# Optimization experiments

Hardware: AMD Instinct MI355X
Metric: run time of the kernel (lower is better)

Reference implementation:

```python
import jax, jax.numpy as jnp
import numpy as np

EMBED_DIM = 512
NUM_HEADS = 8
HEAD_DIM = EMBED_DIM // NUM_HEADS
BATCH = 2
SEQ = 4096
LN_EPS = 1e-5


def setup_inputs() -> dict:
    key = jax.random.key(0)
    ks = jax.random.split(key, 10)
    s = 1.0 / np.sqrt(EMBED_DIM)
    d = dict(
        x=jax.random.normal(ks[0], (BATCH, SEQ, EMBED_DIM), dtype=jnp.float32),
        wq=jax.random.normal(ks[1], (EMBED_DIM, EMBED_DIM), dtype=jnp.float32) * s,
        bq=jnp.zeros((EMBED_DIM,), jnp.float32),
        wk=jax.random.normal(ks[2], (EMBED_DIM, EMBED_DIM), dtype=jnp.float32) * s,
        bk=jnp.zeros((EMBED_DIM,), jnp.float32),
        wv=jax.random.normal(ks[3], (EMBED_DIM, EMBED_DIM), dtype=jnp.float32) * s,
        bv=jnp.zeros((EMBED_DIM,), jnp.float32),
        wo=jax.random.normal(ks[4], (EMBED_DIM, EMBED_DIM), dtype=jnp.float32) * s,
        bo=jnp.zeros((EMBED_DIM,), jnp.float32),
        ln_g=jnp.ones((EMBED_DIM,), jnp.float32),
        ln_b=jnp.zeros((EMBED_DIM,), jnp.float32),
    )
    return d


def reference(x, wq, bq, wk, bk, wv, bv, wo, bo, ln_g, ln_b):
    B, S, E = x.shape
    H, D = NUM_HEADS, HEAD_DIM
    residual = x
    # QKV projections (weights stored [in, out])
    q = (x @ wq + bq).reshape(B, S, H, D).transpose(0, 2, 1, 3)  # [B,H,S,D]
    k = (x @ wk + bk).reshape(B, S, H, D).transpose(0, 2, 1, 3)
    v = (x @ wv + bv).reshape(B, S, H, D).transpose(0, 2, 1, 3)
    # scaled dot-product attention
    scores = jnp.einsum('bhsd,bhtd->bhst', q, k) / jnp.sqrt(jnp.float32(D))
    attn = jax.nn.softmax(scores, axis=-1)
    ctx = jnp.einsum('bhst,bhtd->bhsd', attn, v)  # [B,H,S,D]
    ctx = ctx.transpose(0, 2, 1, 3).reshape(B, S, E)
    # output projection (dropout=0 in eval) + residual + LayerNorm
    out = ctx @ wo + bo
    y = out + residual
    mu = jnp.mean(y, axis=-1, keepdims=True)
    var = jnp.var(y, axis=-1, keepdims=True)
    y = (y - mu) * jax.lax.rsqrt(var + LN_EPS) * ln_g + ln_b
    return y
```

## Files before the change

kernel.cpp:

```cpp
#include <hip/hip_runtime.h>


typedef unsigned short u16;
typedef unsigned int u32;
typedef short bf16x8 __attribute__((ext_vector_type(8)));
typedef float f32x2 __attribute__((ext_vector_type(2)));
typedef float f32x4 __attribute__((ext_vector_type(4)));
typedef float f32x8 __attribute__((ext_vector_type(8)));
typedef float f32x16 __attribute__((ext_vector_type(16)));
typedef unsigned short u16x4 __attribute__((ext_vector_type(4)));
typedef unsigned int u32x2 __attribute__((ext_vector_type(2)));
typedef unsigned int u32x4 __attribute__((ext_vector_type(4)));

#define S_LEN 4096
#define E_DIM 512
#define H_NUM 8
#define D_DIM 64
#define M_ROWS 8192

#define Q_SCALE 0.18033688011112042f

static __device__ __forceinline__ u16 f2bf(float f) {
    unsigned int u = __float_as_uint(f);
    u += 0x7fffu + ((u >> 16) & 1u);
    return (u16)(u >> 16);
}

static __device__ __forceinline__ u32 cvt_pk_bf16(float a, float b) {
    u32 r;
    asm("v_cvt_pk_bf16_f32 %0, %1, %2" : "=v"(r) : "v"(a), "v"(b));
    return r;
}

#if __has_builtin(__builtin_amdgcn_exp2f)
#define EXP2(x) __builtin_amdgcn_exp2f(x)
#else
static __device__ __forceinline__ float exp2_hw(float x) {
    float r;
    asm volatile("v_exp_f32 %0, %1\n\ts_nop 1" : "=v"(r) : "v"(x));
    return r;
}
#define EXP2(x) exp2_hw(x)
#endif

static __device__ __forceinline__ float vsum16(f32x16 v) {
    f32x8 a = __builtin_shufflevector(v, v, 0, 1, 2, 3, 4, 5, 6, 7) +
              __builtin_shufflevector(v, v, 8, 9, 10, 11, 12, 13, 14, 15);
    f32x4 b = __builtin_shufflevector(a, a, 0, 1, 2, 3) +
              __builtin_shufflevector(a, a, 4, 5, 6, 7);
    f32x2 c = __builtin_shufflevector(b, b, 0, 1) +
              __builtin_shufflevector(b, b, 2, 3);
    return c[0] + c[1];
}

static __device__ __forceinline__ void gload_lds16(const u16* g, u16* l) {
    __builtin_amdgcn_global_load_lds(
        (const __attribute__((address_space(1))) u32*)g,
        (__attribute__((address_space(3))) u32*)l, 16, 0, 0);
}

__global__ __launch_bounds__(256) void cvt_all_k(
    const float* __restrict__ x, u16* __restrict__ xb,
    const float* __restrict__ w0, const float* __restrict__ w1,
    const float* __restrict__ w2, const float* __restrict__ w3,
    u16* __restrict__ o0, u16* __restrict__ o1,
    u16* __restrict__ o2, u16* __restrict__ o3)
{
    __shared__ float fT[64][68];
    if (blockIdx.x < 4096) {
        int i = blockIdx.x * 256 + threadIdx.x;
        float4 v = ((const float4*)x)[i];
        u16x4 o;
        o[0] = f2bf(v.x); o[1] = f2bf(v.y); o[2] = f2bf(v.z); o[3] = f2bf(v.w);
        ((u16x4*)xb)[i] = o;
        return;
    }
    const int g = blockIdx.x - 4096;
    const int which = g >> 6;
    const int tile = g & 63;
    const int k0 = (tile >> 3) * 64, n0 = (tile & 7) * 64;
    const float* w = which == 0 ? w0 : which == 1 ? w1 : which == 2 ? w2 : w3;
    u16* o = which == 0 ? o0 : which == 1 ? o1 : which == 2 ? o2 : o3;
    const int tr = threadIdx.x >> 4, tc = threadIdx.x & 15;
    #pragma unroll
    for (int p = 0; p < 4; p++) {
        const int kr = p * 16 + tr;
        float4 v = *(const float4*)&w[(size_t)(k0 + kr) * 512 + n0 + tc * 4];
        fT[tc * 4 + 0][kr] = v.x;
        fT[tc * 4 + 1][kr] = v.y;
        fT[tc * 4 + 2][kr] = v.z;
        fT[tc * 4 + 3][kr] = v.w;
    }
    __syncthreads();
    #pragma unroll
    for (int p = 0; p < 4; p++) {
        const int nr = p * 16 + tr;
        u16x4 ov;
        ov[0] = f2bf(fT[nr][tc * 4 + 0]);
        ov[1] = f2bf(fT[nr][tc * 4 + 1]);
        ov[2] = f2bf(fT[nr][tc * 4 + 2]);
        ov[3] = f2bf(fT[nr][tc * 4 + 3]);
        *(u16x4*)&o[(size_t)(n0 + nr) * 512 + k0 + tc * 4] = ov;
    }
}

template <int BM, int BN>
__global__ __launch_bounds__(256) void qkv_k(
    const u16* __restrict__ A,
    const u16* __restrict__ Wt0, const u16* __restrict__ Wt1,
    const u16* __restrict__ Wt2,
    const float* __restrict__ b0, const float* __restrict__ b1,
    const float* __restrict__ b2,
    u16* __restrict__ q_out, u16* __restrict__ k_out, u16* __restrict__ vt_out)
{
    constexpr int FM = BM / 32, FN = BN / 32;
    __shared__ __align__(16) u16 Asm[BM * 32];
    __shared__ __align__(16) u16 Bsm[BN * 32];

    const int t = threadIdx.x, wave = t >> 6, lane = t & 63;
    constexpr int nb_per = 512 / BN;
    const int sel = blockIdx.x / nb_per, bn = blockIdx.x % nb_per;
    const int bm = blockIdx.y;

    const u16* Wt = sel == 0 ? Wt0 : (sel == 1 ? Wt1 : Wt2);
    const float* bias = sel == 0 ? b0 : (sel == 1 ? b1 : b2);

    const int wm = (wave >> 1) * (BM / 2);
    const int wn = (wave & 1) * (BN / 2);
    const int lrow = lane & 15, kq = (lane >> 4) * 8;

    f32x4 acc[FM][FN];
    #pragma unroll
    for (int i = 0; i < FM; i++)
        #pragma unroll
        for (int j = 0; j < FN; j++)
            acc[i][j] = (f32x4){0.f, 0.f, 0.f, 0.f};

    const u16* Ag = A + (size_t)bm * BM * 512 + (size_t)(t >> 2) * 512 + (t & 3) * 8;
    const u16* Bg = Wt + (size_t)bn * BN * 512 + (size_t)(t >> 2) * 512 + (t & 3) * 8;
    u16* Al = Asm + (size_t)wave * 512;
    u16* Bl = Bsm + (size_t)wave * 512;

    for (int kk = 0; kk < 512; kk += 32) {
        #pragma unroll
        for (int p = 0; p < BM / 64; p++)
            gload_lds16(Ag + (size_t)p * 64 * 512 + kk, Al + p * 2048);
        #pragma unroll
        for (int p = 0; p < BN / 64; p++)
            gload_lds16(Bg + (size_t)p * 64 * 512 + kk, Bl + p * 2048);
        __syncthreads();

        bf16x8 af[FM], bfv[FN];
        #pragma unroll
        for (int i = 0; i < FM; i++)
            af[i] = *(const bf16x8*)&Asm[(wm + i * 16 + lrow) * 32 + kq];
        #pragma unroll
        for (int j = 0; j < FN; j++)
            bfv[j] = *(const bf16x8*)&Bsm[(wn + j * 16 + lrow) * 32 + kq];
        #pragma unroll
        for (int i = 0; i < FM; i++)
            #pragma unroll
            for (int j = 0; j < FN; j++)
                acc[i][j] = __builtin_amdgcn_mfma_f32_16x16x32_bf16(
                    af[i], bfv[j], acc[i][j], 0, 0, 0);
        __syncthreads();
    }

    #pragma unroll
    for (int i = 0; i < FM; i++) {
        #pragma unroll
        for (int j = 0; j < FN; j++) {
            const int col = bn * BN + wn + j * 16 + lrow;
            const float bcol = bias[col];
            const int row0 = bm * BM + wm + i * 16 + (lane >> 4) * 4;
            const int b = row0 >> 12, s0v = row0 & 4095;
            const int h = col >> 6,  d = col & 63;
            if (sel == 2) {
                u16x4 pk;
                #pragma unroll
                for (int q = 0; q < 4; q++)
                    pk[q] = f2bf(acc[i][j][q] + bcol);
                *(u16x4*)&vt_out[(((size_t)(b * 8 + h)) * 64 + d) * 4096 + s0v] = pk;
            } else {
                u16* o = (sel == 0) ? q_out : k_out;
                const float sc = (sel == 0) ? Q_SCALE : 1.0f;
                #pragma unroll
                for (int q = 0; q < 4; q++)
                    o[(((size_t)(b * 8 + h)) * 4096 + s0v + q) * 64 + d] =
                        f2bf((acc[i][j][q] + bcol) * sc);
            }
        }
    }
}

__global__ __launch_bounds__(256) void oproj_ln_k(
    const u16* __restrict__ A,
    const u16* __restrict__ Wt,
    const float* __restrict__ bo,
    const float* __restrict__ x,
    const float* __restrict__ g, const float* __restrict__ beta,
    float* __restrict__ out)
{
    __shared__ __align__(16) u16 Asm[32 * 32];
    __shared__ __align__(16) u16 Bsm[512 * 32];
    __shared__ float red[4][32][2];

    const int t = threadIdx.x, wave = t >> 6, lane = t & 63;
    const int lrow = lane & 15, kq4 = (lane >> 4) * 4, kq = (lane >> 4) * 8;
    const int wn = wave * 128;
    const int bm = blockIdx.x;

    f32x4 acc[2][8];
    #pragma unroll
    for (int i = 0; i < 2; i++)
        #pragma unroll
        for (int j = 0; j < 8; j++)
            acc[i][j] = (f32x4){0.f, 0.f, 0.f, 0.f};

    const u16* Ag = A + (size_t)bm * 32 * 512 + (size_t)(t >> 2) * 512 + (t & 3) * 8;
    const u16* Bg = Wt + (size_t)(t >> 2) * 512 + (t & 3) * 8;
    u16* Al = Asm + (size_t)wave * 512;
    u16* Bl = Bsm + (size_t)wave * 512;

    for (int kk = 0; kk < 512; kk += 32) {
        if (t < 128) gload_lds16(Ag + kk, Al);
        #pragma unroll
        for (int p = 0; p < 8; p++)
            gload_lds16(Bg + (size_t)p * 64 * 512 + kk, Bl + p * 2048);
        __syncthreads();

        bf16x8 af[2], bfv[8];
        #pragma unroll
        for (int i = 0; i < 2; i++)
            af[i] = *(const bf16x8*)&Asm[(i * 16 + lrow) * 32 + kq];
        #pragma unroll
        for (int j = 0; j < 8; j++)
            bfv[j] = *(const bf16x8*)&Bsm[(wn + j * 16 + lrow) * 32 + kq];
        #pragma unroll
        for (int i = 0; i < 2; i++)
            #pragma unroll
            for (int j = 0; j < 8; j++)
                acc[i][j] = __builtin_amdgcn_mfma_f32_16x16x32_bf16(
                    af[i], bfv[j], acc[i][j], 0, 0, 0);
        __syncthreads();
    }

    const int grow0 = bm * 32;
    #pragma unroll
    for (int i = 0; i < 2; i++) {
        #pragma unroll
        for (int q = 0; q < 4; q++) {
            const int rl = i * 16 + kq4 + q;
            float s = 0.f, ss = 0.f;
            #pragma unroll
            for (int j = 0; j < 8; j++) {
                const int col = wn + j * 16 + lrow;
                float v = acc[i][j][q] + bo[col] +
                          x[(size_t)(grow0 + rl) * 512 + col];
                acc[i][j][q] = v;
                s += v; ss += v * v;
            }
            s  += __shfl_xor(s, 1);  ss += __shfl_xor(ss, 1);
            s  += __shfl_xor(s, 2);  ss += __shfl_xor(ss, 2);
            s  += __shfl_xor(s, 4);  ss += __shfl_xor(ss, 4);
            s  += __shfl_xor(s, 8);  ss += __shfl_xor(ss, 8);
            if (lrow == 0) { red[wave][rl][0] = s; red[wave][rl][1] = ss; }
        }
    }
    __syncthreads();

    #pragma unroll
    for (int i = 0; i < 2; i++) {
        #pragma unroll
        for (int q = 0; q < 4; q++) {
            const int rl = i * 16 + kq4 + q;
            const float srow = red[0][rl][0] + red[1][rl][0] +
                               red[2][rl][0] + red[3][rl][0];
            const float ssrow = red[0][rl][1] + red[1][rl][1] +
                                red[2][rl][1] + red[3][rl][1];
            const float mu = srow * (1.0f / 512.0f);
            const float var = ssrow * (1.0f / 512.0f) - mu * mu;
            const float inv = rsqrtf(var + 1e-5f);
            #pragma unroll
            for (int j = 0; j < 8; j++) {
                const int col = wn + j * 16 + lrow;
                out[(size_t)(grow0 + rl) * 512 + col] =
                    (acc[i][j][q] - mu) * inv * g[col] + beta[col];
            }
        }
    }
}

__global__ __launch_bounds__(512, 2) void attn_k(
    const u16* __restrict__ Q, const u16* __restrict__ K,
    const u16* __restrict__ Vt, u16* __restrict__ ctx)
{
    __shared__ __align__(16) u16 SM[32768];

    const int t = threadIdx.x, w = t >> 6, lane = t & 63;
    const int l31 = lane & 31, hi = lane >> 5;
    const int kh = w >> 2, wl = w & 3;

    const int bid = blockIdx.x;
    const int xcd = bid & 7, j = bid >> 3;
    const int head = xcd * 2 + (j & 1);
    const int qt = j >> 1;

    const u16* Qb = Q + (size_t)head * S_LEN * D_DIM;
    const u16* Kb = K + (size_t)head * S_LEN * D_DIM;
    const u16* Vb = Vt + (size_t)head * D_DIM * S_LEN;
    const int q0w = qt * 256 + wl * 64;

    bf16x8 qfA[4], qfB[4];
    #pragma unroll
    for (int ks = 0; ks < 4; ks++) {
        qfA[ks] = *(const bf16x8*)&Qb[(size_t)(q0w + l31) * 64 + ks * 16 + hi * 8];
        qfB[ks] = *(const bf16x8*)&Qb[(size_t)(q0w + 32 + l31) * 64 + ks * 16 + hi * 8];
    }

    u16* const KH = SM + kh * 16384;
    u16* const VH = KH + 8192;

    const u16* kp[8];
    const u16* vp[8];
    #pragma unroll
    for (int i = 0; i < 8; i++) {
        const int r = (i >> 2) * 32 + l31;
        const int c = (i & 3) * 2 + hi;
        const int phys = r * 8 + (c ^ (r & 7));
        kp[i] = KH + phys * 8;
        vp[i] = VH + phys * 8;
    }

    f32x16 acc0A = {0.f}, acc1A = {0.f}, acc0B = {0.f}, acc1B = {0.f};
    float lA = 0.f, lB = 0.f;
    f32x16 sCA, sCB, sNA, sNB;
    bf16x8 pfA[2], pfB[2];

    const int th = t & 255;
    const int c0 = th, c1 = th + 256;
    const int sr0 = c0 >> 3, sc0 = (c0 & 7) ^ (sr0 & 7);
    const int sr1 = c1 >> 3, sc1 = (c1 & 7) ^ (sr1 & 7);
    const u16* kg0 = Kb + (size_t)(kh * 2048 + sr0) * 64 + sc0 * 8;
    const u16* kg1 = Kb + (size_t)(kh * 2048 + sr1) * 64 + sc1 * 8;
    const u16* vg0 = Vb + (size_t)sr0 * S_LEN + kh * 2048 + sc0 * 8;
    const u16* vg1 = Vb + (size_t)sr1 * S_LEN + kh * 2048 + sc1 * 8;
    u16* const kd0 = KH + wl * 512;
    u16* const kd1 = KH + 2048 + wl * 512;
    u16* const vd0 = VH + wl * 512;
    u16* const vd1 = VH + 2048 + wl * 512;

#define ATTN_STAGE(DST)                                                      \
    {                                                                        \
        gload_lds16(kg0, kd0 + (DST)); gload_lds16(kg1, kd1 + (DST));        \
        gload_lds16(vg0, vd0 + (DST)); gload_lds16(vg1, vd1 + (DST));        \
        kg0 += 4096; kg1 += 4096; vg0 += 64; vg1 += 64;                      \
    }

#define QK_H(BUF, H, SA, SB)                                                 \
    {                                                                        \
        SA = (f32x16){0.f}; SB = (f32x16){0.f};                              \
        __builtin_amdgcn_s_setprio(1);                                       \
        _Pragma("unroll")                                                    \
        for (int ks = 0; ks < 4; ks++) {                                     \
            bf16x8 ka = *(const bf16x8*)(kp[4 * (H) + ks] + (BUF));          \
            SA = __builtin_amdgcn_mfma_f32_32x32x16_bf16(ka, qfA[ks], SA, 0, 0, 0); \
            SB = __builtin_amdgcn_mfma_f32_32x32x16_bf16(ka, qfB[ks], SB, 0, 0, 0); \
        }                                                                    \
        __builtin_amdgcn_s_setprio(0);                                       \
    }

#define EXPPACK_H(SA, SB)                                                    \
    {                                                                        \
        _Pragma("unroll")                                                    \
        for (int e = 0; e < 16; e++) {                                       \
            SA[e] = EXP2(SA[e]); SB[e] = EXP2(SB[e]);                        \
        }                                                                    \
        lA += vsum16(SA);                                                    \
        lB += vsum16(SB);                                                    \
        _Pragma("unroll")                                                    \
        for (int jx = 0; jx < 2; jx++) {                                     \
            const int r0 = jx * 8;                                           \
            u32 ax1 = cvt_pk_bf16(SA[r0 + 0], SA[r0 + 1]);                   \
            u32 ay1 = cvt_pk_bf16(SA[r0 + 4], SA[r0 + 5]);                   \
            asm("v_permlane32_swap_b32 %0, %1" : "+v"(ax1), "+v"(ay1));      \
            u32 ax2 = cvt_pk_bf16(SA[r0 + 2], SA[r0 + 3]);                   \
            u32 ay2 = cvt_pk_bf16(SA[r0 + 6], SA[r0 + 7]);                   \
            asm("v_permlane32_swap_b32 %0, %1" : "+v"(ax2), "+v"(ay2));      \
            u32x4 wva; wva[0] = ax1; wva[1] = ax2; wva[2] = ay1; wva[3] = ay2; \
            pfA[jx] = *(bf16x8*)&wva;                                        \
            u32 bx1 = cvt_pk_bf16(SB[r0 + 0], SB[r0 + 1]);                   \
            u32 by1 = cvt_pk_bf16(SB[r0 + 4], SB[r0 + 5]);                   \
            asm("v_permlane32_swap_b32 %0, %1" : "+v"(bx1), "+v"(by1));      \
            u32 bx2 = cvt_pk_bf16(SB[r0 + 2], SB[r0 + 3]);                   \
            u32 by2 = cvt_pk_bf16(SB[r0 + 6], SB[r0 + 7]);                   \
            asm("v_permlane32_swap_b32 %0, %1" : "+v"(bx2), "+v"(by2));      \
            u32x4 wvb; wvb[0] = bx1; wvb[1] = bx2; wvb[2] = by1; wvb[3] = by2; \
            pfB[jx] = *(bf16x8*)&wvb;                                        \
        }                                                                    \
    }

#define PV_H(BUF, H)                                                         \
    {                                                                        \
        __builtin_amdgcn_s_setprio(1);                                       \
        _Pragma("unroll")                                                    \
        for (int jx = 0; jx < 2; jx++) {                                     \
            bf16x8 va = *(const bf16x8*)(vp[2 * (H) + jx] + (BUF));          \
            bf16x8 vb2 = *(const bf16x8*)(vp[4 + 2 * (H) + jx] + (BUF));     \
            acc0A = __builtin_amdgcn_mfma_f32_32x32x16_bf16(va, pfA[jx], acc0A, 0, 0, 0); \
            acc0B = __builtin_amdgcn_mfma_f32_32x32x16_bf16(va, pfB[jx], acc0B, 0, 0, 0); \
            acc1A = __builtin_amdgcn_mfma_f32_32x32x16_bf16(vb2, pfA[jx], acc1A, 0, 0, 0); \
            acc1B = __builtin_amdgcn_mfma_f32_32x32x16_bf16(vb2, pfB[jx], acc1B, 0, 0, 0); \
        }                                                                    \
        __builtin_amdgcn_s_setprio(0);                                       \
    }

#define BODY(BUF, NBUF, LAST)                                                \
    {                                                                        \
        if (!(LAST)) ATTN_STAGE(NBUF);                                       \
        if (w & 1) {                                                         \
            EXPPACK_H(sCA, sCB);                                             \
            QK_H(BUF, 1, sNA, sNB);                                          \
        } else {                                                             \
            QK_H(BUF, 1, sNA, sNB);                                          \
            EXPPACK_H(sCA, sCB);                                             \
        }                                                                    \
        PV_H(BUF, 0);                                                        \
        EXPPACK_H(sNA, sNB);                                                 \
        PV_H(BUF, 1);                                                        \
        __syncthreads();                                                     \
        if (!(LAST)) QK_H(NBUF, 0, sCA, sCB);                                \
    }

    ATTN_STAGE(0);
    __syncthreads();
    QK_H(0, 0, sCA, sCB);

    for (int it = 0; it < 15; ++it) {
        BODY(0, 4096, 0);
        BODY(4096, 0, 0);
    }
    BODY(0, 4096, 0);
    BODY(4096, 0, 1);

    __syncthreads();
    float* const cb = (float*)SM;
    float* const p = cb + (size_t)(wl * 64 + lane) * 34;
    if (kh == 1) {
        #pragma unroll
        for (int e = 0; e < 16; e++) { p[e] = acc0A[e]; p[16 + e] = acc0B[e]; }
        p[32] = lA; p[33] = lB;
    }
    __syncthreads();
    if (kh == 0) {
        #pragma unroll
        for (int e = 0; e < 16; e++) { acc0A[e] += p[e]; acc0B[e] += p[16 + e]; }
        lA += p[32]; lB += p[33];
    }
    __syncthreads();
    if (kh == 1) {
        #pragma unroll
        for (int e = 0; e < 16; e++) { p[e] = acc1A[e]; p[16 + e] = acc1B[e]; }
    }
    __syncthreads();
    if (kh == 0) {
        #pragma unroll
        for (int e = 0; e < 16; e++) { acc1A[e] += p[e]; acc1B[e] += p[16 + e]; }
        lA += __shfl_xor(lA, 32);
        lB += __shfl_xor(lB, 32);

        const int b = head >> 3, h = head & 7;
        const float liA = 1.0f / lA, liB = 1.0f / lB;
        const size_t oA = (size_t)(b * S_LEN + q0w + l31) * 512 + h * 64 + 4 * hi;
        const size_t oB = oA + (size_t)32 * 512;
        #pragma unroll
        for (int rq = 0; rq < 4; rq++) {
            u32x2 wa;
            wa[0] = cvt_pk_bf16(acc0A[4 * rq + 0] * liA, acc0A[4 * rq + 1] * liA);
            wa[1] = cvt_pk_bf16(acc0A[4 * rq + 2] * liA, acc0A[4 * rq + 3] * liA);
            *(u32x2*)&ctx[oA + 8 * rq] = wa;
            wa[0] = cvt_pk_bf16(acc1A[4 * rq + 0] * liA, acc1A[4 * rq + 1] * liA);
            wa[1] = cvt_pk_bf16(acc1A[4 * rq + 2] * liA, acc1A[4 * rq + 3] * liA);
            *(u32x2*)&ctx[oA + 32 + 8 * rq] = wa;
            wa[0] = cvt_pk_bf16(acc0B[4 * rq + 0] * liB, acc0B[4 * rq + 1] * liB);
            wa[1] = cvt_pk_bf16(acc0B[4 * rq + 2] * liB, acc0B[4 * rq + 3] * liB);
            *(u32x2*)&ctx[oB + 8 * rq] = wa;
            wa[0] = cvt_pk_bf16(acc1B[4 * rq + 0] * liB, acc1B[4 * rq + 1] * liB);
            wa[1] = cvt_pk_bf16(acc1B[4 * rq + 2] * liB, acc1B[4 * rq + 3] * liB);
            *(u32x2*)&ctx[oB + 32 + 8 * rq] = wa;
        }
    }
#undef ATTN_STAGE
#undef QK_H
#undef EXPPACK_H
#undef PV_H
#undef BODY
}

extern "C" void kernel_launch(void* const* d_in, const int* in_sizes, int n_in,
                              void* d_out, int out_size, void* d_ws, size_t ws_size,
                              hipStream_t stream)
{
    const float* x    = (const float*)d_in[0];
    const float* wq   = (const float*)d_in[1];
    const float* bq   = (const float*)d_in[2];
    const float* wk   = (const float*)d_in[3];
    const float* bk   = (const float*)d_in[4];
    const float* wv   = (const float*)d_in[5];
    const float* bv   = (const float*)d_in[6];
    const float* wo   = (const float*)d_in[7];
    const float* bo   = (const float*)d_in[8];
    const float* ln_g = (const float*)d_in[9];
    const float* ln_b = (const float*)d_in[10];

    char* ws = (char*)d_ws;
    u16* xb   = (u16*)(ws);
    u16* wqt  = (u16*)(ws + 8388608);
    u16* wkt  = (u16*)(ws + 8912896);
    u16* wvt  = (u16*)(ws + 9437184);
    u16* wot  = (u16*)(ws + 9961472);
    u16* Qb   = (u16*)(ws + 10485760);
    u16* Kb   = (u16*)(ws + 18874368);
    u16* Vtb  = (u16*)(ws + 27262976);
    u16* ctxb = (u16*)(ws + 35651584);

    cvt_all_k<<<4352, 256, 0, stream>>>(x, xb, wq, wk, wv, wo,
                                        wqt, wkt, wvt, wot);

    qkv_k<128, 128><<<dim3(12, 64), 256, 0, stream>>>(
        xb, wqt, wkt, wvt, bq, bk, bv, Qb, Kb, Vtb);

    attn_k<<<256, 512, 0, stream>>>(Qb, Kb, Vtb, ctxb);

    oproj_ln_k<<<256, 256, 0, stream>>>(ctxb, wot, bo, x, ln_g, ln_b,
                                        (float*)d_out);
}
```

Baseline: 140.2 us.

## Halve attention query tile per block and double QKV GEMM k-step

The attention kernel now gives each wave 32 query rows instead of 64 and launches 512 blocks instead of 256. This halves register accumulators and raises parallelism, but K/V tiles are reloaded twice as often per query and the per-wave odd/even interleave of exp and QK is dropped. The QKV GEMM now stages two 32-wide k-chunks per barrier pair, halving the number of syncs at the cost of doubling its LDS footprint. The attention launch bound drops the minimum of two blocks per CU.

```diff
diff --git a/kernel.cpp b/kernel.cpp
--- a/kernel.cpp
+++ b/kernel.cpp
@@ -114,8 +114,8 @@
     u16* __restrict__ q_out, u16* __restrict__ k_out, u16* __restrict__ vt_out)
 {
     constexpr int FM = BM / 32, FN = BN / 32;
-    __shared__ __align__(16) u16 Asm[BM * 32];
-    __shared__ __align__(16) u16 Bsm[BN * 32];
+    __shared__ __align__(16) u16 Asm[2 * BM * 32];
+    __shared__ __align__(16) u16 Bsm[2 * BN * 32];
 
     const int t = threadIdx.x, wave = t >> 6, lane = t & 63;
     constexpr int nb_per = 512 / BN;
@@ -141,28 +141,38 @@
     u16* Al = Asm + (size_t)wave * 512;
     u16* Bl = Bsm + (size_t)wave * 512;
 
-    for (int kk = 0; kk < 512; kk += 32) {
-        #pragma unroll
-        for (int p = 0; p < BM / 64; p++)
-            gload_lds16(Ag + (size_t)p * 64 * 512 + kk, Al + p * 2048);
-        #pragma unroll
-        for (int p = 0; p < BN / 64; p++)
-            gload_lds16(Bg + (size_t)p * 64 * 512 + kk, Bl + p * 2048);
+    for (int kk = 0; kk < 512; kk += 64) {
+        #pragma unroll
+        for (int c = 0; c < 2; c++) {
+            #pragma unroll
+            for (int p = 0; p < BM / 64; p++)
+                gload_lds16(Ag + (size_t)p * 64 * 512 + kk + c * 32,
+                            Al + c * (BM * 32) + p * 2048);
+            #pragma unroll
+            for (int p = 0; p < BN / 64; p++)
+                gload_lds16(Bg + (size_t)p * 64 * 512 + kk + c * 32,
+                            Bl + c * (BN * 32) + p * 2048);
+        }
         __syncthreads();
 
-        bf16x8 af[FM], bfv[FN];
-        #pragma unroll
-        for (int i = 0; i < FM; i++)
-            af[i] = *(const bf16x8*)&Asm[(wm + i * 16 + lrow) * 32 + kq];
-        #pragma unroll
-        for (int j = 0; j < FN; j++)
-            bfv[j] = *(const bf16x8*)&Bsm[(wn + j * 16 + lrow) * 32 + kq];
-        #pragma unroll
-        for (int i = 0; i < FM; i++)
+        #pragma unroll
+        for (int c = 0; c < 2; c++) {
+            bf16x8 af[FM], bfv[FN];
+            #pragma unroll
+            for (int i = 0; i < FM; i++)
+                af[i] = *(const bf16x8*)
+                    &Asm[c * (BM * 32) + (wm + i * 16 + lrow) * 32 + kq];
             #pragma unroll
             for (int j = 0; j < FN; j++)
-                acc[i][j] = __builtin_amdgcn_mfma_f32_16x16x32_bf16(
-                    af[i], bfv[j], acc[i][j], 0, 0, 0);
+                bfv[j] = *(const bf16x8*)
+                    &Bsm[c * (BN * 32) + (wn + j * 16 + lrow) * 32 + kq];
+            #pragma unroll
+            for (int i = 0; i < FM; i++)
+                #pragma unroll
+                for (int j = 0; j < FN; j++)
+                    acc[i][j] = __builtin_amdgcn_mfma_f32_16x16x32_bf16(
+                        af[i], bfv[j], acc[i][j], 0, 0, 0);
+        }
         __syncthreads();
     }
 
@@ -291,7 +301,7 @@
     }
 }
 
-__global__ __launch_bounds__(512, 2) void attn_k(
+__global__ __launch_bounds__(512) void attn_k(
     const u16* __restrict__ Q, const u16* __restrict__ K,
     const u16* __restrict__ Vt, u16* __restrict__ ctx)
 {
@@ -309,14 +319,12 @@
     const u16* Qb = Q + (size_t)head * S_LEN * D_DIM;
     const u16* Kb = K + (size_t)head * S_LEN * D_DIM;
     const u16* Vb = Vt + (size_t)head * D_DIM * S_LEN;
-    const int q0w = qt * 256 + wl * 64;
-
-    bf16x8 qfA[4], qfB[4];
-    #pragma unroll
-    for (int ks = 0; ks < 4; ks++) {
-        qfA[ks] = *(const bf16x8*)&Qb[(size_t)(q0w + l31) * 64 + ks * 16 + hi * 8];
-        qfB[ks] = *(const bf16x8*)&Qb[(size_t)(q0w + 32 + l31) * 64 + ks * 16 + hi * 8];
-    }
+    const int q0w = qt * 128 + wl * 32;
+
+    bf16x8 qf[4];
+    #pragma unroll
+    for (int ks = 0; ks < 4; ks++)
+        qf[ks] = *(const bf16x8*)&Qb[(size_t)(q0w + l31) * 64 + ks * 16 + hi * 8];
 
     u16* const KH = SM + kh * 16384;
     u16* const VH = KH + 8192;
@@ -332,10 +340,10 @@
         vp[i] = VH + phys * 8;
     }
 
-    f32x16 acc0A = {0.f}, acc1A = {0.f}, acc0B = {0.f}, acc1B = {0.f};
-    float lA = 0.f, lB = 0.f;
-    f32x16 sCA, sCB, sNA, sNB;
-    bf16x8 pfA[2], pfB[2];
+    f32x16 acc0 = {0.f}, acc1 = {0.f};
+    float l = 0.f;
+    f32x16 sC, sN;
+    bf16x8 pf[2];
 
     const int th = t & 255;
     const int c0 = th, c1 = th + 256;
@@ -357,46 +365,34 @@
         kg0 += 4096; kg1 += 4096; vg0 += 64; vg1 += 64;                      \
     }
 
-#define QK_H(BUF, H, SA, SB)                                                 \
+#define QK_H(BUF, H, S)                                                      \
     {                                                                        \
-        SA = (f32x16){0.f}; SB = (f32x16){0.f};                              \
+        S = (f32x16){0.f};                                                   \
         __builtin_amdgcn_s_setprio(1);                                       \
         _Pragma("unroll")                                                    \
         for (int ks = 0; ks < 4; ks++) {                                     \
             bf16x8 ka = *(const bf16x8*)(kp[4 * (H) + ks] + (BUF));          \
-            SA = __builtin_amdgcn_mfma_f32_32x32x16_bf16(ka, qfA[ks], SA, 0, 0, 0); \
-            SB = __builtin_amdgcn_mfma_f32_32x32x16_bf16(ka, qfB[ks], SB, 0, 0, 0); \
+            S = __builtin_amdgcn_mfma_f32_32x32x16_bf16(ka, qf[ks], S, 0, 0, 0); \
         }                                                                    \
         __builtin_amdgcn_s_setprio(0);                                       \
     }
 
-#define EXPPACK_H(SA, SB)                                                    \
+#define EXPPACK_H(S)                                                         \
     {                                                                        \
         _Pragma("unroll")                                                    \
-        for (int e = 0; e < 16; e++) {                                       \
-            SA[e] = EXP2(SA[e]); SB[e] = EXP2(SB[e]);                        \
-        }                                                                    \
-        lA += vsum16(SA);                                                    \
-        lB += vsum16(SB);                                                    \
+        for (int e = 0; e < 16; e++) S[e] = EXP2(S[e]);                      \
+        l += vsum16(S);                                                      \
         _Pragma("unroll")                                                    \
         for (int jx = 0; jx < 2; jx++) {                                     \
             const int r0 = jx * 8;                                           \
-            u32 ax1 = cvt_pk_bf16(SA[r0 + 0], SA[r0 + 1]);                   \
-            u32 ay1 = cvt_pk_bf16(SA[r0 + 4], SA[r0 + 5]);                   \
-            asm("v_permlane32_swap_b32 %0, %1" : "+v"(ax1), "+v"(ay1));      \
-            u32 ax2 = cvt_pk_bf16(SA[r0 + 2], SA[r0 + 3]);                   \
-            u32 ay2 = cvt_pk_bf16(SA[r0 + 6], SA[r0 + 7]);                   \
-            asm("v_permlane32_swap_b32 %0, %1" : "+v"(ax2), "+v"(ay2));      \
-            u32x4 wva; wva[0] = ax1; wva[1] = ax2; wva[2] = ay1; wva[3] = ay2; \
-            pfA[jx] = *(bf16x8*)&wva;                                        \
-            u32 bx1 = cvt_pk_bf16(SB[r0 + 0], SB[r0 + 1]);                   \
-            u32 by1 = cvt_pk_bf16(SB[r0 + 4], SB[r0 + 5]);                   \
-            asm("v_permlane32_swap_b32 %0, %1" : "+v"(bx1), "+v"(by1));      \
-            u32 bx2 = cvt_pk_bf16(SB[r0 + 2], SB[r0 + 3]);                   \
-            u32 by2 = cvt_pk_bf16(SB[r0 + 6], SB[r0 + 7]);                   \
-            asm("v_permlane32_swap_b32 %0, %1" : "+v"(bx2), "+v"(by2));      \
-            u32x4 wvb; wvb[0] = bx1; wvb[1] = bx2; wvb[2] = by1; wvb[3] = by2; \
-            pfB[jx] = *(bf16x8*)&wvb;                                        \
+            u32 x1 = cvt_pk_bf16(S[r0 + 0], S[r0 + 1]);                      \
+            u32 y1 = cvt_pk_bf16(S[r0 + 4], S[r0 + 5]);                      \
+            asm("v_permlane32_swap_b32 %0, %1" : "+v"(x1), "+v"(y1));        \
+            u32 x2 = cvt_pk_bf16(S[r0 + 2], S[r0 + 3]);                      \
+            u32 y2 = cvt_pk_bf16(S[r0 + 6], S[r0 + 7]);                      \
+            asm("v_permlane32_swap_b32 %0, %1" : "+v"(x2), "+v"(y2));        \
+            u32x4 wv; wv[0] = x1; wv[1] = x2; wv[2] = y1; wv[3] = y2;        \
+            pf[jx] = *(bf16x8*)&wv;                                          \
         }                                                                    \
     }
 
@@ -407,10 +403,8 @@
         for (int jx = 0; jx < 2; jx++) {                                     \
             bf16x8 va = *(const bf16x8*)(vp[2 * (H) + jx] + (BUF));          \
             bf16x8 vb2 = *(const bf16x8*)(vp[4 + 2 * (H) + jx] + (BUF));     \
-            acc0A = __builtin_amdgcn_mfma_f32_32x32x16_bf16(va, pfA[jx], acc0A, 0, 0, 0); \
-            acc0B = __builtin_amdgcn_mfma_f32_32x32x16_bf16(va, pfB[jx], acc0B, 0, 0, 0); \
-            acc1A = __builtin_amdgcn_mfma_f32_32x32x16_bf16(vb2, pfA[jx], acc1A, 0, 0, 0); \
-            acc1B = __builtin_amdgcn_mfma_f32_32x32x16_bf16(vb2, pfB[jx], acc1B, 0, 0, 0); \
+            acc0 = __builtin_amdgcn_mfma_f32_32x32x16_bf16(va, pf[jx], acc0, 0, 0, 0); \
+            acc1 = __builtin_amdgcn_mfma_f32_32x32x16_bf16(vb2, pf[jx], acc1, 0, 0, 0); \
         }                                                                    \
         __builtin_amdgcn_s_setprio(0);                                       \
     }
@@ -418,23 +412,18 @@
 #define BODY(BUF, NBUF, LAST)                                                \
     {                                                                        \
         if (!(LAST)) ATTN_STAGE(NBUF);                                       \
-        if (w & 1) {                                                         \
-            EXPPACK_H(sCA, sCB);                                             \
-            QK_H(BUF, 1, sNA, sNB);                                          \
-        } else {                                                             \
-            QK_H(BUF, 1, sNA, sNB);                                          \
-            EXPPACK_H(sCA, sCB);                                             \
-        }                                                                    \
+        QK_H(BUF, 1, sN);                                                    \
+        EXPPACK_H(sC);                                                       \
         PV_H(BUF, 0);                                                        \
-        EXPPACK_H(sNA, sNB);                                                 \
+        EXPPACK_H(sN);                                                       \
         PV_H(BUF, 1);                                                        \
         __syncthreads();                                                     \
-        if (!(LAST)) QK_H(NBUF, 0, sCA, sCB);                                \
+        if (!(LAST)) QK_H(NBUF, 0, sC);                                      \
     }
 
     ATTN_STAGE(0);
     __syncthreads();
-    QK_H(0, 0, sCA, sCB);
+    QK_H(0, 0, sC);
 
     for (int it = 0; it < 15; ++it) {
         BODY(0, 4096, 0);
@@ -445,49 +434,31 @@
 
     __syncthreads();
     float* const cb = (float*)SM;
-    float* const p = cb + (size_t)(wl * 64 + lane) * 34;
+    float* const p = cb + (size_t)(wl * 64 + lane) * 33;
     if (kh == 1) {
         #pragma unroll
-        for (int e = 0; e < 16; e++) { p[e] = acc0A[e]; p[16 + e] = acc0B[e]; }
-        p[32] = lA; p[33] = lB;
+        for (int e = 0; e < 16; e++) { p[e] = acc0[e]; p[16 + e] = acc1[e]; }
+        p[32] = l;
     }
     __syncthreads();
     if (kh == 0) {
         #pragma unroll
-        for (int e = 0; e < 16; e++) { acc0A[e] += p[e]; acc0B[e] += p[16 + e]; }
-        lA += p[32]; lB += p[33];
-    }
-    __syncthreads();
-    if (kh == 1) {
-        #pragma unroll
-        for (int e = 0; e < 16; e++) { p[e] = acc1A[e]; p[16 + e] = acc1B[e]; }
-    }
-    __syncthreads();
-    if (kh == 0) {
-        #pragma unroll
-        for (int e = 0; e < 16; e++) { acc1A[e] += p[e]; acc1B[e] += p[16 + e]; }
-        lA += __shfl_xor(lA, 32);
-        lB += __shfl_xor(lB, 32);
+        for (int e = 0; e < 16; e++) { acc0[e] += p[e]; acc1[e] += p[16 + e]; }
+        l += p[32];
+        l += __shfl_xor(l, 32);
 
         const int b = head >> 3, h = head & 7;
-        const float liA = 1.0f / lA, liB = 1.0f / lB;
-        const size_t oA = (size_t)(b * S_LEN + q0w + l31) * 512 + h * 64 + 4 * hi;
-        const size_t oB = oA + (size_t)32 * 512;
+        const float li = 1.0f / l;
+        const size_t o = (size_t)(b * S_LEN + q0w + l31) * 512 + h * 64 + 4 * hi;
         #pragma unroll
         for (int rq = 0; rq < 4; rq++) {
             u32x2 wa;
-            wa[0] = cvt_pk_bf16(acc0A[4 * rq + 0] * liA, acc0A[4 * rq + 1] * liA);
-            wa[1] = cvt_pk_bf16(acc0A[4 * rq + 2] * liA, acc0A[4 * rq + 3] * liA);
-            *(u32x2*)&ctx[oA + 8 * rq] = wa;
-            wa[0] = cvt_pk_bf16(acc1A[4 * rq + 0] * liA, acc1A[4 * rq + 1] * liA);
-            wa[1] = cvt_pk_bf16(acc1A[4 * rq + 2] * liA, acc1A[4 * rq + 3] * liA);
-            *(u32x2*)&ctx[oA + 32 + 8 * rq] = wa;
-            wa[0] = cvt_pk_bf16(acc0B[4 * rq + 0] * liB, acc0B[4 * rq + 1] * liB);
-            wa[1] = cvt_pk_bf16(acc0B[4 * rq + 2] * liB, acc0B[4 * rq + 3] * liB);
-            *(u32x2*)&ctx[oB + 8 * rq] = wa;
-            wa[0] = cvt_pk_bf16(acc1B[4 * rq + 0] * liB, acc1B[4 * rq + 1] * liB);
-            wa[1] = cvt_pk_bf16(acc1B[4 * rq + 2] * liB, acc1B[4 * rq + 3] * liB);
-            *(u32x2*)&ctx[oB + 32 + 8 * rq] = wa;
+            wa[0] = cvt_pk_bf16(acc0[4 * rq + 0] * li, acc0[4 * rq + 1] * li);
+            wa[1] = cvt_pk_bf16(acc0[4 * rq + 2] * li, acc0[4 * rq + 3] * li);
+            *(u32x2*)&ctx[o + 8 * rq] = wa;
+            wa[0] = cvt_pk_bf16(acc1[4 * rq + 0] * li, acc1[4 * rq + 1] * li);
+            wa[1] = cvt_pk_bf16(acc1[4 * rq + 2] * li, acc1[4 * rq + 3] * li);
+            *(u32x2*)&ctx[o + 32 + 8 * rq] = wa;
         }
     }
 #undef ATTN_STAGE
@@ -530,7 +501,7 @@
     qkv_k<128, 128><<<dim3(12, 64), 256, 0, stream>>>(
         xb, wqt, wkt, wvt, bq, bk, bv, Qb, Kb, Vtb);
 
-    attn_k<<<256, 512, 0, stream>>>(Qb, Kb, Vtb, ctxb);
+    attn_k<<<512, 512, 0, stream>>>(Qb, Kb, Vtb, ctxb);
 
     oproj_ln_k<<<256, 256, 0, stream>>>(ctxb, wot, bo, x, ln_g, ln_b,
                                         (float*)d_out);
```

Measured after the change: 143.6 us. 1.02x slower.
